# Optimization experiments

Measured on AMD Instinct MI355X. Metric: run time of the kernel, lower is better.

Reference implementation:

```python
import jax, jax.numpy as jnp
import numpy as np

N_NODES = 100000
N_EDGES = 1200000
D_IN = 64
D_OUT = 32
BN_EPS = 1e-5


def setup_inputs() -> dict:
    key = jax.random.key(0)
    ks = jax.random.split(key, 8)
    x = jax.random.normal(ks[0], (N_NODES, D_IN), dtype=jnp.float32)
    edge_index = jax.random.randint(ks[1], (2, N_EDGES), 0, N_NODES, dtype=jnp.int64)
    W1s = jax.random.normal(ks[2], (3, D_IN, D_IN), dtype=jnp.float32) * 0.05
    b1s = jax.random.normal(ks[3], (3, D_IN), dtype=jnp.float32) * 0.05
    W2s = jax.random.normal(ks[4], (3, D_IN, D_IN), dtype=jnp.float32) * 0.05
    b2s = jax.random.normal(ks[5], (3, D_IN), dtype=jnp.float32) * 0.05
    gammas = jnp.ones((3, D_IN), dtype=jnp.float32)
    betas = jnp.zeros((3, D_IN), dtype=jnp.float32)
    epss = jnp.zeros((3,), dtype=jnp.float32)  # GINConv train_eps init value 0
    lin_w = jax.random.normal(ks[6], (D_IN, D_OUT), dtype=jnp.float32) * 0.05
    lin_b = jnp.zeros((D_OUT,), dtype=jnp.float32)
    return {"x": x, "edge_index": edge_index, "W1s": W1s, "b1s": b1s,
            "W2s": W2s, "b2s": b2s, "gammas": gammas, "betas": betas,
            "epss": epss, "lin_w": lin_w, "lin_b": lin_b}


def reference(x, edge_index, W1s, b1s, W2s, b2s, gammas, betas, epss, lin_w, lin_b):
    # PyG GINConv (source_to_target): out_i = nn((1+eps)*x_i + sum_{j->i} x_j)
    src = edge_index[0]
    dst = edge_index[1]
    n = x.shape[0]
    h = x
    for i in range(3):
        agg = jax.ops.segment_sum(h[src], dst, num_segments=n)  # [N, d]
        z = (1.0 + epss[i]) * h + agg
        z = jax.nn.relu(z @ W1s[i] + b1s[i])
        z = jax.nn.relu(z @ W2s[i] + b2s[i])
        # BatchNorm1d, training mode (batch statistics, biased variance)
        mu = jnp.mean(z, axis=0)
        var = jnp.var(z, axis=0)
        z = gammas[i] * (z - mu) * jax.lax.rsqrt(var + BN_EPS) + betas[i]
        h = jax.nn.relu(z)  # F.relu after each conv
    return h @ lin_w + lin_b  # [N, D_OUT]
```

## Files before the change

### kernel.cpp

```cpp
#include <hip/hip_runtime.h>
#include <hip/hip_fp16.h>

#define NBMAX 256
#define BCAP  8192
#define CHB   3584

typedef _Float16 half8 __attribute__((ext_vector_type(8)));
typedef float f32x4 __attribute__((ext_vector_type(4)));

__device__ __forceinline__ unsigned short f2h(float f) {
    __half h = __float2half_rn(f);
    return *(unsigned short*)&h;
}

__device__ __forceinline__ int scan256(int v, int* wsum, int* woff) {
    int t = threadIdx.x, lane = t & 63, wv = t >> 6;
    int x = v;
    #pragma unroll
    for (int d = 1; d < 64; d <<= 1) {
        int y = __shfl_up(x, d, 64);
        if (lane >= d) x += y;
    }
    if (lane == 63) wsum[wv] = x;
    __syncthreads();
    if (t == 0) {
        int a = 0;
        #pragma unroll
        for (int i = 0; i < 4; ++i) { woff[i] = a; a += wsum[i]; }
    }
    __syncthreads();
    return x - v + woff[wv];
}

__global__ __launch_bounds__(256) void gin_x16init(const float* __restrict__ x,
                                                   unsigned short* __restrict__ o, int n16,
                                                   const void* __restrict__ edge,
                                                   int* __restrict__ flag,
                                                   int* __restrict__ gcount, int nb,
                                                   float* __restrict__ stats, int E) {
    if (blockIdx.x == gridDim.x - 1) {
        int t = threadIdx.x;
        for (int i = t; i < nb; i += 256) gcount[i] = 0;
        for (int i = t; i < 384; i += 256) stats[i] = 0.f;
        if (t == 0) {
            const int* p = (const int*)edge;
            int is64 = 1;
            int m = (E < 64) ? E : 64;
            for (int i = 0; i < m; ++i)
                if (p[2 * i + 1] != 0) is64 = 0;
            *flag = is64;
        }
        return;
    }
    int i = blockIdx.x * 256 + threadIdx.x;
    if (i >= n16) return;
    float4 v = ((const float4*)x)[i];
    ushort4 u;
    u.x = f2h(v.x); u.y = f2h(v.y); u.z = f2h(v.z); u.w = f2h(v.w);
    ((ushort4*)o)[i] = u;
}

__global__ __launch_bounds__(256) void gin_binscatter(const void* __restrict__ edge,
                                                      const int* __restrict__ flag,
                                                      int* __restrict__ gcount,
                                                      uint2* __restrict__ ebuf, int E, int nb) {
    __shared__ int cnt[NBMAX];
    __shared__ int dlt[NBMAX];
    __shared__ int cur[NBMAX];
    __shared__ int wsum[4], woff[4];
    __shared__ uint2 buf[CHB];
    int t = threadIdx.x;
    int beg = blockIdx.x * CHB;
    int m = E - beg; if (m > CHB) m = CHB;
    if (t < nb) cnt[t] = 0;
    __syncthreads();
    int is64 = *flag;
    for (int j = t; j < m; j += 256) {
        int e = beg + j;
        int d = is64 ? (int)((const long long*)edge)[E + e] : ((const int*)edge)[E + e];
        atomicAdd(&cnt[d >> 9], 1);
    }
    __syncthreads();
    int v = (t < nb) ? cnt[t] : 0;
    int excl = scan256(v, wsum, woff);
    if (t < nb) {
        int gb = v ? atomicAdd(&gcount[t], v) : 0;
        dlt[t] = t * BCAP + gb - excl;
        cur[t] = excl;
    }
    __syncthreads();
    for (int j = t; j < m; j += 256) {
        int e = beg + j;
        int s, d;
        if (is64) {
            s = (int)((const long long*)edge)[e];
            d = (int)((const long long*)edge)[E + e];
        } else {
            s = ((const int*)edge)[e];
            d = ((const int*)edge)[E + e];
        }
        int p = atomicAdd(&cur[d >> 9], 1);
        buf[p] = make_uint2((unsigned)s, (unsigned)d);
    }
    __syncthreads();
    for (int j = t; j < m; j += 256) {
        uint2 ed = buf[j];
        ebuf[j + dlt[(int)(ed.y >> 9)]] = ed;
    }
}

__global__ __launch_bounds__(256) void gin_build(const uint2* __restrict__ ebuf,
                                                 const int* __restrict__ gcount,
                                                 int* __restrict__ rowbeg,
                                                 int* __restrict__ rowend,
                                                 int* __restrict__ col, int n) {
    __shared__ int cnt[512];
    __shared__ int off[512];
    __shared__ int wsum[4], woff[4];
    int b = blockIdx.x, t = threadIdx.x;
    int beg = b * BCAP;
    int end = beg + gcount[b];
    cnt[t] = 0; cnt[t + 256] = 0;
    __syncthreads();
    for (int j = beg + t; j < end; j += 256)
        atomicAdd(&cnt[(int)(ebuf[j].y & 511)], 1);
    __syncthreads();
    int v0 = cnt[2 * t], v1 = cnt[2 * t + 1];
    int ep = scan256(v0 + v1, wsum, woff);
    off[2 * t] = ep;
    off[2 * t + 1] = ep + v0;
    __syncthreads();
    int node0 = b * 512 + 2 * t;
    if (node0 < n) {
        rowbeg[node0] = beg + off[2 * t];
        rowend[node0] = beg + off[2 * t] + v0;
    }
    if (node0 + 1 < n) {
        rowbeg[node0 + 1] = beg + off[2 * t + 1];
        rowend[node0 + 1] = beg + off[2 * t + 1] + v1;
    }
    __syncthreads();
    for (int j = beg + t; j < end; j += 256) {
        uint2 ed = ebuf[j];
        int p = atomicAdd(&off[(int)(ed.y & 511)], 1);
        col[beg + p] = (int)ed.x;
    }
}

template <bool APPLY>
__device__ __forceinline__ void accum8(float* acc, uint4 u,
                                       const float* sc, const float* sh) {
    float v[8];
    float2 f;
    f = __half22float2(*(const __half2*)&u.x); v[0] = f.x; v[1] = f.y;
    f = __half22float2(*(const __half2*)&u.y); v[2] = f.x; v[3] = f.y;
    f = __half22float2(*(const __half2*)&u.z); v[4] = f.x; v[5] = f.y;
    f = __half22float2(*(const __half2*)&u.w); v[6] = f.x; v[7] = f.y;
    #pragma unroll
    for (int j = 0; j < 8; ++j)
        acc[j] += APPLY ? fmaxf(fmaf(v[j], sc[j], sh[j]), 0.f) : v[j];
}

template <bool APPLY>
__device__ __forceinline__ void gather_node(const unsigned short* __restrict__ zb,
                                            int r0, int r1,
                                            const int* __restrict__ col,
                                            float e1,
                                            const float* sc, const float* sh,
                                            _Float16* __restrict__ trow,
                                            int wid, int qn, int l16) {
    int r = l16 >> 3, c = l16 & 7;
    uint4 su = make_uint4(0, 0, 0, 0);
    if (r == 0) su = *(const uint4*)(zb + (size_t)wid * 64 + 8 * c);

    float acc[8] = {0.f, 0.f, 0.f, 0.f, 0.f, 0.f, 0.f, 0.f};
    for (int b2 = r0; b2 < r1; b2 += 16) {
        int ce = b2 + l16;
        int ci = col[ce < r1 ? ce : r1 - 1];
        uint4 u[8];
        bool p[8];
        #pragma unroll
        for (int s = 0; s < 8; ++s) {
            int j = 2 * s + r;
            p[s] = (b2 + j) < r1;
            int idx = __shfl(ci, 16 * qn + j);
            if (p[s]) u[s] = *(const uint4*)(zb + (size_t)idx * 64 + 8 * c);
        }
        #pragma unroll
        for (int s = 0; s < 8; ++s)
            if (p[s]) accum8<APPLY>(acc, u[s], sc, sh);
    }
    #pragma unroll
    for (int j = 0; j < 8; ++j)
        acc[j] += __shfl_xor(acc[j], 8);
    if (r == 0) {
        float s[8];
        float2 f;
        f = __half22float2(*(const __half2*)&su.x); s[0] = f.x; s[1] = f.y;
        f = __half22float2(*(const __half2*)&su.y); s[2] = f.x; s[3] = f.y;
        f = __half22float2(*(const __half2*)&su.z); s[4] = f.x; s[5] = f.y;
        f = __half22float2(*(const __half2*)&su.w); s[6] = f.x; s[7] = f.y;
        #pragma unroll
        for (int j = 0; j < 8; ++j) {
            float v = APPLY ? fmaxf(fmaf(s[j], sc[j], sh[j]), 0.f) : s[j];
            acc[j] = fmaf(e1, v, acc[j]);
        }
        uint4 o;
        o.x = (unsigned)f2h(acc[0]) | ((unsigned)f2h(acc[1]) << 16);
        o.y = (unsigned)f2h(acc[2]) | ((unsigned)f2h(acc[3]) << 16);
        o.z = (unsigned)f2h(acc[4]) | ((unsigned)f2h(acc[5]) << 16);
        o.w = (unsigned)f2h(acc[6]) | ((unsigned)f2h(acc[7]) << 16);
        *(uint4*)(trow + 8 * c) = o;
    }
}

template <bool APPLY>
__global__ __launch_bounds__(256, 4) void gin_fused(const unsigned short* __restrict__ zb,
                                                    const int* __restrict__ rowbeg,
                                                    const int* __restrict__ rowend,
                                                    const int* __restrict__ col,
                                                    const float* __restrict__ epss,
                                                    const float* __restrict__ gammas,
                                                    const float* __restrict__ betas,
                                                    float fN,
                                                    unsigned short* __restrict__ z16,
                                                    const float* __restrict__ W1g,
                                                    const float* __restrict__ b1g,
                                                    const float* __restrict__ W2g,
                                                    const float* __restrict__ b2g,
                                                    float* __restrict__ stats,
                                                    int layer, int n) {
    __shared__ _Float16 Wt[2 * 64 * 72];
    __shared__ _Float16 Tz[128 * 72];
    __shared__ float sS[64], sQ[64];
    __shared__ float sBN[128];
    int tid = threadIdx.x;
    int base = blockIdx.x * 128;
    const float* __restrict__ W1 = W1g + layer * 4096;
    const float* __restrict__ W2 = W2g + layer * 4096;

    for (int i = tid; i < 4096; i += 256) {
        int k = i >> 6, nn = i & 63;
        Wt[nn * 72 + k]        = (_Float16)W1[i];
        Wt[4608 + nn * 72 + k] = (_Float16)W2[i];
    }
    if (tid < 64) {
        sS[tid] = 0.f; sQ[tid] = 0.f;
        if (APPLY) {
            float mu  = stats[(layer - 1) * 128 + tid] / fN;
            float var = stats[(layer - 1) * 128 + 64 + tid] / fN - mu * mu;
            float g   = gammas[(layer - 1) * 64 + tid];
            float grs = g * rsqrtf(var + 1e-5f);
            sBN[tid]      = grs;
            sBN[64 + tid] = betas[(layer - 1) * 64 + tid] - grs * mu;
        }
    }
    __syncthreads();

    int lane = tid & 63, wv = tid >> 6;
    int qn = lane >> 4;
    int l16 = lane & 15;
    int c8 = l16 & 7;
    float e1 = 1.f + epss[layer];
    float sc[8] = {1.f, 1.f, 1.f, 1.f, 1.f, 1.f, 1.f, 1.f};
    float sh[8] = {0.f, 0.f, 0.f, 0.f, 0.f, 0.f, 0.f, 0.f};
    if (APPLY) {
        *(float4*)&sc[0] = *(const float4*)&sBN[8 * c8];
        *(float4*)&sc[4] = *(const float4*)&sBN[8 * c8 + 4];
        *(float4*)&sh[0] = *(const float4*)&sBN[64 + 8 * c8];
        *(float4*)&sh[4] = *(const float4*)&sBN[64 + 8 * c8 + 4];
    }

    int wid0 = base + wv * 4 + qn;
    int nr0 = 0, nr1 = 0;
    if (wid0 < n) { nr0 = rowbeg[wid0]; nr1 = rowend[wid0]; }
    #pragma unroll 1
    for (int p = 0; p < 8; ++p) {
        int widl = p * 16 + wv * 4 + qn;
        int wid = base + widl;
        int r0 = nr0, r1 = nr1;
        if (p < 7) {
            int w2 = wid + 16;
            nr0 = 0; nr1 = 0;
            if (w2 < n) { nr0 = rowbeg[w2]; nr1 = rowend[w2]; }
        }
        if (wid < n) {
            gather_node<APPLY>(zb, r0, r1, col, e1, sc, sh,
                               Tz + widl * 72, wid, qn, l16);
        } else if (l16 < 8) {
            *(uint4*)(Tz + widl * 72 + 8 * c8) = make_uint4(0u, 0u, 0u, 0u);
        }
    }
    __syncthreads();

    int g = qn, q = l16;
    int n0 = 32 * wv + q;
    int n1 = n0 + 16;

    half8 tb00 = *(const half8*)&Tz[n0 * 72 + 8 * g];
    half8 tb01 = *(const half8*)&Tz[n0 * 72 + 32 + 8 * g];
    half8 tb10 = *(const half8*)&Tz[n1 * 72 + 8 * g];
    half8 tb11 = *(const half8*)&Tz[n1 * 72 + 32 + 8 * g];

    f32x4 acc[2][4];
    #pragma unroll
    for (int nt = 0; nt < 2; ++nt)
        #pragma unroll
        for (int ft = 0; ft < 4; ++ft)
            acc[nt][ft] = (f32x4){0.f, 0.f, 0.f, 0.f};

    #pragma unroll
    for (int ft = 0; ft < 4; ++ft) {
        half8 a0 = *(const half8*)&Wt[(16 * ft + q) * 72 + 8 * g];
        half8 a1 = *(const half8*)&Wt[(16 * ft + q) * 72 + 32 + 8 * g];
        acc[0][ft] = __builtin_amdgcn_mfma_f32_16x16x32_f16(a0, tb00, acc[0][ft], 0, 0, 0);
        acc[0][ft] = __builtin_amdgcn_mfma_f32_16x16x32_f16(a1, tb01, acc[0][ft], 0, 0, 0);
        acc[1][ft] = __builtin_amdgcn_mfma_f32_16x16x32_f16(a0, tb10, acc[1][ft], 0, 0, 0);
        acc[1][ft] = __builtin_amdgcn_mfma_f32_16x16x32_f16(a1, tb11, acc[1][ft], 0, 0, 0);
    }

    #pragma unroll
    for (int ft = 0; ft < 4; ++ft) {
        float4 b = *(const float4*)(b1g + layer * 64 + 16 * ft + 4 * g);
        #pragma unroll
        for (int nt = 0; nt < 2; ++nt) {
            int node = nt ? n1 : n0;
            float v0 = fmaxf(acc[nt][ft][0] + b.x, 0.f);
            float v1 = fmaxf(acc[nt][ft][1] + b.y, 0.f);
            float v2 = fmaxf(acc[nt][ft][2] + b.z, 0.f);
            float v3 = fmaxf(acc[nt][ft][3] + b.w, 0.f);
            uint2 pk;
            pk.x = (unsigned)f2h(v0) | ((unsigned)f2h(v1) << 16);
            pk.y = (unsigned)f2h(v2) | ((unsigned)f2h(v3) << 16);
            *(uint2*)&Tz[node * 72 + 16 * ft + 4 * g] = pk;
        }
    }

    half8 zb00 = *(const half8*)&Tz[n0 * 72 + 8 * g];
    half8 zb01 = *(const half8*)&Tz[n0 * 72 + 32 + 8 * g];
    half8 zb10 = *(const half8*)&Tz[n1 * 72 + 8 * g];
    half8 zb11 = *(const half8*)&Tz[n1 * 72 + 32 + 8 * g];
    #pragma unroll
    for (int nt = 0; nt < 2; ++nt)
        #pragma unroll
        for (int ft = 0; ft < 4; ++ft)
            acc[nt][ft] = (f32x4){0.f, 0.f, 0.f, 0.f};
    #pragma unroll
    for (int ft = 0; ft < 4; ++ft) {
        half8 a0 = *(const half8*)&Wt[4608 + (16 * ft + q) * 72 + 8 * g];
        half8 a1 = *(const half8*)&Wt[4608 + (16 * ft + q) * 72 + 32 + 8 * g];
        acc[0][ft] = __builtin_amdgcn_mfma_f32_16x16x32_f16(a0, zb00, acc[0][ft], 0, 0, 0);
        acc[0][ft] = __builtin_amdgcn_mfma_f32_16x16x32_f16(a1, zb01, acc[0][ft], 0, 0, 0);
        acc[1][ft] = __builtin_amdgcn_mfma_f32_16x16x32_f16(a0, zb10, acc[1][ft], 0, 0, 0);
        acc[1][ft] = __builtin_amdgcn_mfma_f32_16x16x32_f16(a1, zb11, acc[1][ft], 0, 0, 0);
    }

    #pragma unroll
    for (int ft = 0; ft < 4; ++ft) {
        float4 b = *(const float4*)(b2g + layer * 64 + 16 * ft + 4 * g);
        float s[4] = {0.f, 0.f, 0.f, 0.f};
        float sq[4] = {0.f, 0.f, 0.f, 0.f};
        #pragma unroll
        for (int nt = 0; nt < 2; ++nt) {
            int node = base + (nt ? n1 : n0);
            float v0 = fmaxf(acc[nt][ft][0] + b.x, 0.f);
            float v1 = fmaxf(acc[nt][ft][1] + b.y, 0.f);
            float v2 = fmaxf(acc[nt][ft][2] + b.z, 0.f);
            float v3 = fmaxf(acc[nt][ft][3] + b.w, 0.f);
            if (node < n) {
                s[0] += v0; sq[0] += v0 * v0;
                s[1] += v1; sq[1] += v1 * v1;
                s[2] += v2; sq[2] += v2 * v2;
                s[3] += v3; sq[3] += v3 * v3;
                uint2 pk;
                pk.x = (unsigned)f2h(v0) | ((unsigned)f2h(v1) << 16);
                pk.y = (unsigned)f2h(v2) | ((unsigned)f2h(v3) << 16);
                *(uint2*)(z16 + (size_t)node * 64 + 16 * ft + 4 * g) = pk;
            }
        }
        #pragma unroll
        for (int off = 1; off < 16; off <<= 1) {
            #pragma unroll
            for (int r2 = 0; r2 < 4; ++r2) {
                s[r2] += __shfl_xor(s[r2], off);
                sq[r2] += __shfl_xor(sq[r2], off);
            }
        }
        if (q == 0) {
            #pragma unroll
            for (int r2 = 0; r2 < 4; ++r2) {
                atomicAdd(&sS[16 * ft + 4 * g + r2], s[r2]);
                atomicAdd(&sQ[16 * ft + 4 * g + r2], sq[r2]);
            }
        }
    }
    __syncthreads();
    if (tid < 64) {
        atomicAdd(&stats[layer * 128 + tid], sS[tid]);
        atomicAdd(&stats[layer * 128 + 64 + tid], sQ[tid]);
    }
}

__global__ __launch_bounds__(256) void gin_lin(const unsigned short* __restrict__ zin,
                                               const float* __restrict__ stats,
                                               const float* __restrict__ gammas,
                                               const float* __restrict__ betas,
                                               float fN,
                                               const float* __restrict__ lw,
                                               const float* __restrict__ lb,
                                               float* __restrict__ out, int n) {
    __shared__ float Z[128 * 68];
    int tid = threadIdx.x;
    int base = blockIdx.x * 128;
    int cq = (tid & 15) * 4;
    float4 sc4, sh4;
    {
        float t0[4], t1[4];
        #pragma unroll
        for (int j = 0; j < 4; ++j) {
            int f = cq + j;
            float mu  = stats[256 + f] / fN;
            float var = stats[256 + 64 + f] / fN - mu * mu;
            float g   = gammas[128 + f];
            float grs = g * rsqrtf(var + 1e-5f);
            t0[j] = grs;
            t1[j] = betas[128 + f] - grs * mu;
        }
        sc4 = make_float4(t0[0], t0[1], t0[2], t0[3]);
        sh4 = make_float4(t1[0], t1[1], t1[2], t1[3]);
    }
    {
        const ushort4* __restrict__ src = (const ushort4*)(zin + (size_t)base * 64);
        #pragma unroll
        for (int it = 0; it < 8; ++it) {
            int idx4 = it * 256 + tid;
            int row = idx4 >> 4, c = (idx4 & 15) * 4;
            float4 v = make_float4(0.f, 0.f, 0.f, 0.f);
            if (base + row < n) {
                ushort4 u = src[idx4];
                float2 f0 = __half22float2(*(const __half2*)&u.x);
                float2 f1 = __half22float2(*(const __half2*)&u.z);
                v = make_float4(f0.x, f0.y, f1.x, f1.y);
            }
            float4 r;
            r.x = fmaxf(fmaf(v.x, sc4.x, sh4.x), 0.f);
            r.y = fmaxf(fmaf(v.y, sc4.y, sh4.y), 0.f);
            r.z = fmaxf(fmaf(v.z, sc4.z, sh4.z), 0.f);
            r.w = fmaxf(fmaf(v.w, sc4.w, sh4.w), 0.f);
            *(float4*)&Z[row * 68 + c] = r;
        }
    }
    __syncthreads();
    int tx = tid & 7, ty = tid >> 3;
    float acc[4][4];
    {
        float4 b = *(const float4*)(lb + 4 * tx);
        #pragma unroll
        for (int r = 0; r < 4; ++r) {
            acc[r][0] = b.x; acc[r][1] = b.y; acc[r][2] = b.z; acc[r][3] = b.w;
        }
    }
    #pragma unroll 4
    for (int k = 0; k < 64; ++k) {
        float4 w = *(const float4*)(lw + k * 32 + 4 * tx);
        #pragma unroll
        for (int r = 0; r < 4; ++r) {
            float a = Z[(ty + 32 * r) * 68 + k];
            acc[r][0] = fmaf(a, w.x, acc[r][0]);
            acc[r][1] = fmaf(a, w.y, acc[r][1]);
            acc[r][2] = fmaf(a, w.z, acc[r][2]);
            acc[r][3] = fmaf(a, w.w, acc[r][3]);
        }
    }
    #pragma unroll
    for (int r = 0; r < 4; ++r) {
        int row = base + ty + 32 * r;
        if (row < n) {
            float4 v;
            v.x = acc[r][0]; v.y = acc[r][1]; v.z = acc[r][2]; v.w = acc[r][3];
            *(float4*)(out + (size_t)row * 32 + 4 * tx) = v;
        }
    }
}

extern "C" void kernel_launch(void* const* d_in, const int* in_sizes, int n_in,
                              void* d_out, int out_size, void* d_ws, size_t ws_size,
                              hipStream_t stream) {
    const float* x      = (const float*)d_in[0];
    const void*  edge   = d_in[1];
    const float* W1s    = (const float*)d_in[2];
    const float* b1s    = (const float*)d_in[3];
    const float* W2s    = (const float*)d_in[4];
    const float* b2s    = (const float*)d_in[5];
    const float* gammas = (const float*)d_in[6];
    const float* betas  = (const float*)d_in[7];
    const float* epss   = (const float*)d_in[8];
    const float* lin_w  = (const float*)d_in[9];
    const float* lin_b  = (const float*)d_in[10];
    float* out = (float*)d_out;

    const int N = in_sizes[0] / 64;
    const int E = in_sizes[1] / 2;
    const int NB = (N + 511) >> 9;
    const float fN = (float)N;

    char* w = (char*)d_ws;
    auto take = [&](size_t bytes) {
        char* p = w;
        w += (bytes + 255) & ~(size_t)255;
        return p;
    };
    unsigned short* x16 = (unsigned short*)take((size_t)N * 64 * 2);
    unsigned short* hA  = (unsigned short*)take((size_t)N * 64 * 2);
    unsigned short* hB  = (unsigned short*)take((size_t)N * 64 * 2);
    uint2* ebuf    = (uint2*)take((size_t)NB * BCAP * 8);
    int*   col     = (int*)take((size_t)NB * BCAP * 4);
    int*   rowbeg  = (int*)take((size_t)N * 4);
    int*   rowend  = (int*)take((size_t)N * 4);
    int*   gcount  = (int*)take((size_t)NBMAX * 4);
    float* stats   = (float*)take(3 * 128 * 4);
    int*   flag    = (int*)take(4);

    const int n16 = N * 16;
    gin_x16init<<<(n16 + 255) / 256 + 1, 256, 0, stream>>>(x, x16, n16, edge, flag,
                                                           gcount, NB, stats, E);
    gin_binscatter<<<(E + CHB - 1) / CHB, 256, 0, stream>>>(edge, flag, gcount, ebuf, E, NB);
    gin_build<<<NB, 256, 0, stream>>>(ebuf, gcount, rowbeg, rowend, col, N);

    const int gMlp = (N + 127) / 128;
    const unsigned short* zin = x16;
    unsigned short* zout = hA;
    for (int L = 0; L < 3; ++L) {
        if (L == 0)
            gin_fused<false><<<gMlp, 256, 0, stream>>>(zin, rowbeg, rowend, col, epss,
                                                       gammas, betas, fN, zout,
                                                       W1s, b1s, W2s, b2s, stats, L, N);
        else
            gin_fused<true><<<gMlp, 256, 0, stream>>>(zin, rowbeg, rowend, col, epss,
                                                      gammas, betas, fN, zout,
                                                      W1s, b1s, W2s, b2s, stats, L, N);
        zin = zout;
        zout = (zout == hA) ? hB : hA;
    }
    gin_lin<<<gMlp, 256, 0, stream>>>(zin, stats, gammas, betas, fN, lin_w, lin_b, out, N);
}
```

Measured before the change: 294.7 us.

## Halve weight LDS to raise occupancy and prefetch CSR rows two nodes ahead

Measured after the change: 318.0 us. +7.9%, slower.

```diff
diff --git a/kernel.cpp b/kernel.cpp
--- a/kernel.cpp
+++ b/kernel.cpp
@@ -163,7 +163,7 @@
 
 template <bool APPLY>
 __device__ __forceinline__ void gather_node(const unsigned short* __restrict__ zb,
-                                            int r0, int r1,
+                                            int r0, int r1, int ci0,
                                             const int* __restrict__ col,
                                             float e1,
                                             const float* sc, const float* sh,
@@ -174,9 +174,12 @@
     if (r == 0) su = *(const uint4*)(zb + (size_t)wid * 64 + 8 * c);
 
     float acc[8] = {0.f, 0.f, 0.f, 0.f, 0.f, 0.f, 0.f, 0.f};
+    int ci = ci0;
     for (int b2 = r0; b2 < r1; b2 += 16) {
-        int ce = b2 + l16;
-        int ci = col[ce < r1 ? ce : r1 - 1];
+        if (b2 > r0) {
+            int ce = b2 + l16;
+            ci = col[ce < r1 ? ce : r1 - 1];
+        }
         uint4 u[8];
         bool p[8];
         #pragma unroll
@@ -215,7 +218,7 @@
 }
 
 template <bool APPLY>
-__global__ __launch_bounds__(256, 4) void gin_fused(const unsigned short* __restrict__ zb,
+__global__ __launch_bounds__(256, 5) void gin_fused(const unsigned short* __restrict__ zb,
                                                     const int* __restrict__ rowbeg,
                                                     const int* __restrict__ rowend,
                                                     const int* __restrict__ col,
@@ -230,7 +233,7 @@
                                                     const float* __restrict__ b2g,
                                                     float* __restrict__ stats,
                                                     int layer, int n) {
-    __shared__ _Float16 Wt[2 * 64 * 72];
+    __shared__ _Float16 Wt[64 * 72];
     __shared__ _Float16 Tz[128 * 72];
     __shared__ float sS[64], sQ[64];
     __shared__ float sBN[128];
@@ -241,8 +244,7 @@
 
     for (int i = tid; i < 4096; i += 256) {
         int k = i >> 6, nn = i & 63;
-        Wt[nn * 72 + k]        = (_Float16)W1[i];
-        Wt[4608 + nn * 72 + k] = (_Float16)W2[i];
+        Wt[nn * 72 + k] = (_Float16)W1[i];
     }
     if (tid < 64) {
         sS[tid] = 0.f; sQ[tid] = 0.f;
@@ -271,25 +273,37 @@
         *(float4*)&sh[4] = *(const float4*)&sBN[64 + 8 * c8 + 4];
     }
 
-    int wid0 = base + wv * 4 + qn;
-    int nr0 = 0, nr1 = 0;
-    if (wid0 < n) { nr0 = rowbeg[wid0]; nr1 = rowend[wid0]; }
+    int wvq = wv * 4 + qn;
+    int cr0, cr1, pr0, pr1;
+    {
+        int w0 = base + wvq;
+        cr0 = 0; cr1 = 0;
+        if (w0 < n) { cr0 = rowbeg[w0]; cr1 = rowend[w0]; }
+        int w1 = w0 + 16;
+        pr0 = 0; pr1 = 0;
+        if (w1 < n) { pr0 = rowbeg[w1]; pr1 = rowend[w1]; }
+    }
+    int cci = 0;
+    if (cr1 > cr0) { int ce = cr0 + l16; cci = col[ce < cr1 ? ce : cr1 - 1]; }
     #pragma unroll 1
     for (int p = 0; p < 8; ++p) {
-        int widl = p * 16 + wv * 4 + qn;
+        int nci = 0;
+        if (pr1 > pr0) { int ce = pr0 + l16; nci = col[ce < pr1 ? ce : pr1 - 1]; }
+        int fr0 = 0, fr1 = 0;
+        {
+            int w2 = base + (p + 2) * 16 + wvq;
+            if (p < 6 && w2 < n) { fr0 = rowbeg[w2]; fr1 = rowend[w2]; }
+        }
+        int widl = p * 16 + wvq;
         int wid = base + widl;
-        int r0 = nr0, r1 = nr1;
-        if (p < 7) {
-            int w2 = wid + 16;
-            nr0 = 0; nr1 = 0;
-            if (w2 < n) { nr0 = rowbeg[w2]; nr1 = rowend[w2]; }
-        }
         if (wid < n) {
-            gather_node<APPLY>(zb, r0, r1, col, e1, sc, sh,
+            gather_node<APPLY>(zb, cr0, cr1, cci, col, e1, sc, sh,
                                Tz + widl * 72, wid, qn, l16);
         } else if (l16 < 8) {
             *(uint4*)(Tz + widl * 72 + 8 * c8) = make_uint4(0u, 0u, 0u, 0u);
         }
+        cr0 = pr0; cr1 = pr1; cci = nci;
+        pr0 = fr0; pr1 = fr1;
     }
     __syncthreads();
 
@@ -336,6 +350,13 @@
         }
     }
 
+    __syncthreads();
+    for (int i = tid; i < 4096; i += 256) {
+        int k = i >> 6, nn = i & 63;
+        Wt[nn * 72 + k] = (_Float16)W2[i];
+    }
+    __syncthreads();
+
     half8 zb00 = *(const half8*)&Tz[n0 * 72 + 8 * g];
     half8 zb01 = *(const half8*)&Tz[n0 * 72 + 32 + 8 * g];
     half8 zb10 = *(const half8*)&Tz[n1 * 72 + 8 * g];
@@ -347,8 +368,8 @@
             acc[nt][ft] = (f32x4){0.f, 0.f, 0.f, 0.f};
     #pragma unroll
     for (int ft = 0; ft < 4; ++ft) {
-        half8 a0 = *(const half8*)&Wt[4608 + (16 * ft + q) * 72 + 8 * g];
-        half8 a1 = *(const half8*)&Wt[4608 + (16 * ft + q) * 72 + 32 + 8 * g];
+        half8 a0 = *(const half8*)&Wt[(16 * ft + q) * 72 + 8 * g];
+        half8 a1 = *(const half8*)&Wt[(16 * ft + q) * 72 + 32 + 8 * g];
         acc[0][ft] = __builtin_amdgcn_mfma_f32_16x16x32_f16(a0, zb00, acc[0][ft], 0, 0, 0);
         acc[0][ft] = __builtin_amdgcn_mfma_f32_16x16x32_f16(a1, zb01, acc[0][ft], 0, 0, 0);
         acc[1][ft] = __builtin_amdgcn_mfma_f32_16x16x32_f16(a0, zb10, acc[1][ft], 0, 0, 0);
```
